# Optimization experiments

Hardware: AMD Instinct MI355X
Metric: run time of the kernel (lower is better)

## Reference

```python
import jax, jax.numpy as jnp
import numpy as np

D_MODEL = 1024
N_HEADS = 16
D_K = D_MODEL // N_HEADS


def setup_inputs() -> dict:
    key = jax.random.key(0)
    ks = jax.random.split(key, 11)
    B, S = 2, 2048
    scale = 0.02
    inp = {
        "q": jax.random.normal(ks[0], (B, S, D_MODEL), jnp.float32),
        "k": jax.random.normal(ks[1], (B, S, D_MODEL), jnp.float32),
        "v": jax.random.normal(ks[2], (B, S, D_MODEL), jnp.float32),
        "w_q": jax.random.normal(ks[3], (D_MODEL, D_MODEL), jnp.float32) * scale,
        "b_q": jnp.zeros((D_MODEL,), jnp.float32),
        "w_k": jax.random.normal(ks[4], (D_MODEL, D_MODEL), jnp.float32) * scale,
        "b_k": jnp.zeros((D_MODEL,), jnp.float32),
        "w_v": jax.random.normal(ks[5], (D_MODEL, D_MODEL), jnp.float32) * scale,
        "b_v": jnp.zeros((D_MODEL,), jnp.float32),
        "w_o": jax.random.normal(ks[6], (D_MODEL, D_MODEL), jnp.float32) * scale,
        "b_o": jnp.zeros((D_MODEL,), jnp.float32),
    }
    return inp


def reference(q, k, v, w_q, b_q, w_k, b_k, w_v, b_v, w_o, b_o):
    B, S, _ = q.shape
    # projections (torch Linear: x @ W.T + b); split into heads -> [B, H, S, d]
    def proj(x, w, b):
        return (x @ w.T + b).reshape(B, S, N_HEADS, D_K).transpose(0, 2, 1, 3)
    qh = proj(q, w_q, b_q)
    kh = proj(k, w_k, b_k)
    vh = proj(v, w_v, b_v)
    scores = jnp.einsum("bhqd,bhkd->bhqk", qh, kh) / jnp.sqrt(
        jnp.asarray(D_K, jnp.float32))
    attn = jax.nn.softmax(scores, axis=-1)  # dropout = identity (eval)
    out = jnp.einsum("bhqk,bhkd->bhqd", attn, vh)
    out = out.transpose(0, 2, 1, 3).reshape(B, S, D_MODEL)
    return out @ w_o.T + b_o
```

## Files before the change

kernel.cpp:

```cpp
#include <hip/hip_runtime.h>

typedef unsigned short u16;
typedef unsigned int u32;
typedef __attribute__((ext_vector_type(4))) unsigned short u16x4;
typedef __attribute__((ext_vector_type(8))) unsigned short u16x8;
typedef __attribute__((ext_vector_type(8))) __bf16 bf16x8;
typedef __attribute__((ext_vector_type(4))) float f32x4;
typedef __attribute__((ext_vector_type(16))) float f32x16;

#define SEQ 2048
#define DMODEL 1024
#define LDP 3072
#define MM (DMODEL * DMODEL)
#define SC 0.18033688f

__device__ __forceinline__ u16 f2bf(float f) {
  unsigned u = __builtin_bit_cast(unsigned, f);
  u = (u + 0x7fffu + ((u >> 16) & 1u)) >> 16;
  return (u16)u;
}

__device__ __forceinline__ u32 cvtpk(float lo, float hi) {
  u32 r;
  asm volatile("v_cvt_pk_bf16_f32 %0, %1, %2" : "=v"(r) : "v"(lo), "v"(hi));
  return r;
}

__device__ __forceinline__ float fexp2(float x) {
#if __has_builtin(__builtin_amdgcn_exp2f)
  return __builtin_amdgcn_exp2f(x);
#else
  return exp2f(x);
#endif
}

__device__ __forceinline__ bf16x8 ldbf8(const u16* p) {
  return __builtin_bit_cast(bf16x8, *(const u16x8*)p);
}
__device__ __forceinline__ bf16x8 ldbf8c(const char* p) {
  return __builtin_bit_cast(bf16x8, *(const u16x8*)p);
}

__device__ __forceinline__ f32x4 mfma16(bf16x8 a, bf16x8 b, f32x4 c) {
  return __builtin_amdgcn_mfma_f32_16x16x32_bf16(a, b, c, 0, 0, 0);
}
__device__ __forceinline__ f32x16 mfma32(bf16x8 a, bf16x8 b, f32x16 c) {
  return __builtin_amdgcn_mfma_f32_32x32x16_bf16(a, b, c, 0, 0, 0);
}

__device__ __forceinline__ void gl16(const void* g, void* l) {
  __builtin_amdgcn_global_load_lds(
      (__attribute__((address_space(1))) void*)(size_t)g,
      (__attribute__((address_space(3))) void*)l, 16, 0, 0);
}

__global__ void cast_all_k(const float* __restrict__ q, const float* __restrict__ k,
                           const float* __restrict__ v, const float* __restrict__ wq,
                           const float* __restrict__ wk, const float* __restrict__ wv,
                           const float* __restrict__ wo, u16* __restrict__ dq,
                           u16* __restrict__ dk, u16* __restrict__ dv,
                           u16* __restrict__ wqkv, u16* __restrict__ wob) {
  int b = blockIdx.x;
  const float* s;
  u16* d;
  if (b < 6144) {
    const int z = b >> 11;
    s = z == 0 ? q : z == 1 ? k : v;
    d = z == 0 ? dq : z == 1 ? dk : dv;
    b &= 2047;
  } else {
    const int z = (b - 6144) >> 9;
    s = z == 0 ? wq : z == 1 ? wk : z == 2 ? wv : wo;
    d = z < 3 ? wqkv + (size_t)z * MM : wob;
    b = (b - 6144) & 511;
  }
  const size_t i = ((size_t)b * blockDim.x + threadIdx.x) * 8;
  const float4 a = *(const float4*)(s + i);
  const float4 c = *(const float4*)(s + i + 4);
  u16x8 o;
  o[0] = f2bf(a.x); o[1] = f2bf(a.y); o[2] = f2bf(a.z); o[3] = f2bf(a.w);
  o[4] = f2bf(c.x); o[5] = f2bf(c.y); o[6] = f2bf(c.z); o[7] = f2bf(c.w);
  *(u16x8*)(d + i) = o;
}

template <int OMODE>
__device__ __forceinline__ void gemm_bt_body(const u16* __restrict__ A,
                                             const u16* __restrict__ Bw,
                                             const float* __restrict__ bias,
                                             void* __restrict__ Cv, const int K,
                                             const int ldc, const int ncol0,
                                             const int m0, const int n0,
                                             const float osc) {
  __shared__ u16 As[128 * 32];
  __shared__ u16 Bs[128 * 32];
  const int tid = threadIdx.x;
  const int lane = tid & 63;
  const int w = tid >> 6;
  const int l15 = lane & 15;
  const int lg = lane >> 4;

  f32x4 acc[4][4] = {};

  const int arow = (w >> 1) * 64 + l15;
  const int brow = (w & 1) * 64 + l15;
  const int kfb = lg * 16;

  const int strow = w * 32 + (lane >> 2);
  const u16* Ag = A + (size_t)(m0 + strow) * K + (lane & 3) * 8;
  const u16* Bg = Bw + (size_t)(n0 + strow) * K + (lane & 3) * 8;
  const size_t rstep = (size_t)16 * K;
  char* AsL0 = (char*)As + w * 32 * 64;
  char* AsL1 = AsL0 + 16 * 64;
  char* BsL0 = (char*)Bs + w * 32 * 64;
  char* BsL1 = BsL0 + 16 * 64;

  for (int k0 = 0; k0 < K; k0 += 32) {
    __syncthreads();
    gl16(Ag + k0, AsL0);
    gl16(Ag + k0 + rstep, AsL1);
    gl16(Bg + k0, BsL0);
    gl16(Bg + k0 + rstep, BsL1);
    __syncthreads();
    bf16x8 af[4], bfv[4];
#pragma unroll
    for (int t = 0; t < 4; ++t) {
      af[t] = ldbf8c((char*)As + (arow + t * 16) * 64 + kfb);
      bfv[t] = ldbf8c((char*)Bs + (brow + t * 16) * 64 + kfb);
    }
    __builtin_amdgcn_s_setprio(1);
#pragma unroll
    for (int i = 0; i < 4; ++i)
#pragma unroll
      for (int j = 0; j < 4; ++j) acc[i][j] = mfma16(af[i], bfv[j], acc[i][j]);
    __builtin_amdgcn_s_setprio(0);
  }

  const int mrow = (w >> 1) * 64 + lg * 4;
  const int ncol = (w & 1) * 64 + l15;
#pragma unroll
  for (int j = 0; j < 4; ++j) {
    const int gn = n0 + ncol + j * 16;
    const float bia = bias[gn];
#pragma unroll
    for (int i = 0; i < 4; ++i) {
      const int gmb = m0 + mrow + i * 16;
#pragma unroll
      for (int r = 0; r < 4; ++r) {
        const float val = (acc[i][j][r] + bia) * osc;
        const int gm = gmb + r;
        if (OMODE == 0) {
          ((float*)Cv)[(size_t)gm * ldc + gn] = val;
        } else if (OMODE == 1) {
          ((u16*)Cv)[(size_t)gm * ldc + ncol0 + gn] = f2bf(val);
        } else {
          const int bb = gm >> 11, ss = gm & 2047;
          const int hh = gn >> 6, dd = gn & 63;
          ((u16*)Cv)[(((size_t)(bb * 16 + hh) * 64 + dd) << 11) + ss] = f2bf(val);
        }
      }
    }
  }
}

__global__ __launch_bounds__(256, 3) void gemm_qkv_k(
    const u16* __restrict__ qb, const u16* __restrict__ kb,
    const u16* __restrict__ vb, const u16* __restrict__ wqkv,
    const float* __restrict__ bq, const float* __restrict__ bk,
    const float* __restrict__ bv, u16* __restrict__ proj, u16* __restrict__ vtb) {
  const int b = blockIdx.x;
  const int xcd = b & 7;
  const int i = b >> 3;
  const int z = i >> 5;
  const int j = i & 31;
  const int m0 = (xcd * 4 + (j >> 3)) * 128;
  const int n0 = (j & 7) * 128;
  if (z == 2)
    gemm_bt_body<2>(vb, wqkv + 2 * (size_t)MM, bv, vtb, DMODEL, 0, 0, m0, n0,
                    1.0f);
  else
    gemm_bt_body<1>(z == 0 ? qb : kb, wqkv + (size_t)z * MM, z == 0 ? bq : bk,
                    proj, DMODEL, LDP, z * DMODEL, m0, n0, z == 0 ? SC : 1.0f);
}

__global__ __launch_bounds__(256, 3) void gemm_o_k(const u16* __restrict__ attnb,
                                                   const u16* __restrict__ wob,
                                                   const float* __restrict__ bo,
                                                   float* __restrict__ out) {
  const int b = blockIdx.x;
  const int xcd = b & 7;
  const int i = b >> 3;
  const int m0 = (xcd * 4 + (i >> 3)) * 128;
  const int n0 = (i & 7) * 128;
  gemm_bt_body<0>(attnb, wob, bo, out, DMODEL, DMODEL, 0, m0, n0, 1.0f);
}

__global__ __launch_bounds__(256, 2) void attn_k(const u16* __restrict__ proj,
                                                 const u16* __restrict__ vtb,
                                                 u16* __restrict__ outa) {
  __shared__ u16 ks[2][64 * 64];
  __shared__ u16 vs[2][64 * 64];
  const int b = blockIdx.x;
  const int slot = b >> 3;
  const int bh = (b & 7) * 4 + (slot >> 4);
  const int qB = (slot & 15) * 128;
  const int tid = threadIdx.x;
  const int lane = tid & 63;
  const int w = tid >> 6;
  const size_t rb = (size_t)(bh >> 4) * SEQ;
  const int h = bh & 15;
  const int l31 = lane & 31;
  const int hi = lane >> 5;
  const int swzk = (l31 & 7) << 4;
  const int swzv = (l31 & 15) << 3;

  const u16* qp = proj + (rb + qB + w * 32 + l31) * LDP + h * 64 + hi * 8;
  bf16x8 qf[4];
#pragma unroll
  for (int km = 0; km < 4; ++km) qf[km] = ldbf8(qp + km * 16);

  const int srow = tid >> 2;
  const int scol = (tid & 3) * 32;
  const int scel = scol >> 1;
  const int kz0 = srow * 128 + (scol ^ ((srow & 7) << 4));
  const int kz1 = srow * 128 + ((scol + 16) ^ ((srow & 7) << 4));
  const int vz0 = srow * 128 + (scol ^ ((srow & 15) << 3));
  const int vz1 = srow * 128 + ((scol + 8) ^ ((srow & 15) << 3));
  const int vz2 = srow * 128 + ((scol + 16) ^ ((srow & 15) << 3));
  const int vz3 = srow * 128 + ((scol + 24) ^ ((srow & 15) << 3));
  const u16* kg = proj + rb * LDP + DMODEL + h * 64;
  const u16* vg = vtb + (size_t)bh * 64 * SEQ;

  u16x8 ka0, ka1, va0, va1;
  {
    const u16* kr = kg + (size_t)srow * LDP + scel;
    ka0 = *(const u16x8*)kr;
    ka1 = *(const u16x8*)(kr + 8);
    const u16* vr = vg + (size_t)srow * SEQ + scel;
    va0 = *(const u16x8*)vr;
    va1 = *(const u16x8*)(vr + 8);
  }

  f32x16 oa0 = {}, oa1 = {};
  float lrun = 0.f;
  int p = 0;

  for (int kv0 = 0; kv0 < SEQ; kv0 += 64) {
    {
      char* kd = (char*)ks[p];
      char* vd = (char*)vs[p];
      *(u16x8*)(kd + kz0) = ka0;
      *(u16x8*)(kd + kz1) = ka1;
      *(u16x4*)(vd + vz0) = *(u16x4*)&va0;
      *(u16x4*)(vd + vz1) = *((u16x4*)&va0 + 1);
      *(u16x4*)(vd + vz2) = *(u16x4*)&va1;
      *(u16x4*)(vd + vz3) = *((u16x4*)&va1 + 1);
    }
    __syncthreads();
    if (kv0 + 64 < SEQ) {
      const u16* kr = kg + (size_t)(kv0 + 64 + srow) * LDP + scel;
      ka0 = *(const u16x8*)kr;
      ka1 = *(const u16x8*)(kr + 8);
      const u16* vr = vg + (size_t)srow * SEQ + kv0 + 64 + scel;
      va0 = *(const u16x8*)vr;
      va1 = *(const u16x8*)(vr + 8);
    }
    const char* kp = (const char*)ks[p];
    const char* vp = (const char*)vs[p];
    f32x16 s0 = {}, s1 = {};
    __builtin_amdgcn_s_setprio(1);
#pragma unroll
    for (int km = 0; km < 4; ++km) {
      const int co = (km * 32 + hi * 16) ^ swzk;
      const bf16x8 k0 = ldbf8c(kp + l31 * 128 + co);
      const bf16x8 k1 = ldbf8c(kp + (32 + l31) * 128 + co);
      s0 = mfma32(k0, qf[km], s0);
      s1 = mfma32(k1, qf[km], s1);
    }
    __builtin_amdgcn_s_setprio(0);

#pragma unroll
    for (int r = 0; r < 16; ++r) s0[r] = fexp2(s0[r]);
#pragma unroll
    for (int r = 0; r < 16; ++r) s1[r] = fexp2(s1[r]);
    float rs = (((s0[0] + s0[1]) + (s0[2] + s0[3])) +
                ((s0[4] + s0[5]) + (s0[6] + s0[7]))) +
               (((s0[8] + s0[9]) + (s0[10] + s0[11])) +
                ((s0[12] + s0[13]) + (s0[14] + s0[15])));
    rs += (((s1[0] + s1[1]) + (s1[2] + s1[3])) +
           ((s1[4] + s1[5]) + (s1[6] + s1[7]))) +
          (((s1[8] + s1[9]) + (s1[10] + s1[11])) +
           ((s1[12] + s1[13]) + (s1[14] + s1[15])));
    rs += __shfl_xor(rs, 32);
    lrun += rs;

    __builtin_amdgcn_s_setprio(1);
#define PCHUNK(SV, G, CB)                                                \
    {                                                                    \
      u16x8 pbu;                                                         \
      ((u32*)&pbu)[0] = cvtpk(SV[G + 0], SV[G + 1]);                     \
      ((u32*)&pbu)[1] = cvtpk(SV[G + 2], SV[G + 3]);                     \
      ((u32*)&pbu)[2] = cvtpk(SV[G + 4], SV[G + 5]);                     \
      ((u32*)&pbu)[3] = cvtpk(SV[G + 6], SV[G + 7]);                     \
      const bf16x8 pb = __builtin_bit_cast(bf16x8, pbu);                 \
      const int vc0 = ((CB) + 8 * hi) ^ swzv;                            \
      const int vc1 = ((CB) + 16 + 8 * hi) ^ swzv;                       \
      const char* vr0 = vp + l31 * 128;                                  \
      const char* vr1 = vp + (32 + l31) * 128;                           \
      u16x8 vf0, vf1;                                                    \
      *(u16x4*)&vf0       = *(const u16x4*)(vr0 + vc0);                  \
      *((u16x4*)&vf0 + 1) = *(const u16x4*)(vr0 + vc1);                  \
      *(u16x4*)&vf1       = *(const u16x4*)(vr1 + vc0);                  \
      *((u16x4*)&vf1 + 1) = *(const u16x4*)(vr1 + vc1);                  \
      oa0 = mfma32(__builtin_bit_cast(bf16x8, vf0), pb, oa0);            \
      oa1 = mfma32(__builtin_bit_cast(bf16x8, vf1), pb, oa1);            \
    }
    PCHUNK(s0, 0, 0)
    PCHUNK(s0, 8, 32)
    PCHUNK(s1, 0, 64)
    PCHUNK(s1, 8, 96)
#undef PCHUNK
    __builtin_amdgcn_s_setprio(0);
    p ^= 1;
  }

  const float invl = 1.0f / lrun;
  u16* orow = outa + (rb + qB + w * 32 + l31) * DMODEL + h * 64 + hi * 4;
#pragma unroll
  for (int g = 0; g < 4; ++g) {
    u16x4 st0, st1;
    ((u32*)&st0)[0] = cvtpk(oa0[4 * g + 0] * invl, oa0[4 * g + 1] * invl);
    ((u32*)&st0)[1] = cvtpk(oa0[4 * g + 2] * invl, oa0[4 * g + 3] * invl);
    *(u16x4*)(orow + 8 * g) = st0;
    ((u32*)&st1)[0] = cvtpk(oa1[4 * g + 0] * invl, oa1[4 * g + 1] * invl);
    ((u32*)&st1)[1] = cvtpk(oa1[4 * g + 2] * invl, oa1[4 * g + 3] * invl);
    *(u16x4*)(orow + 32 + 8 * g) = st1;
  }
}

extern "C" void kernel_launch(void* const* d_in, const int* in_sizes, int n_in,
                              void* d_out, int out_size, void* d_ws, size_t ws_size,
                              hipStream_t stream) {
  const float* q  = (const float*)d_in[0];
  const float* k  = (const float*)d_in[1];
  const float* v  = (const float*)d_in[2];
  const float* wq = (const float*)d_in[3];
  const float* bq = (const float*)d_in[4];
  const float* wk = (const float*)d_in[5];
  const float* bk = (const float*)d_in[6];
  const float* wv = (const float*)d_in[7];
  const float* bv = (const float*)d_in[8];
  const float* wo = (const float*)d_in[9];
  const float* bo = (const float*)d_in[10];

  const size_t NTOK = (size_t)2 * SEQ;
  const size_t NELE = NTOK * DMODEL;
  u16* qb    = (u16*)d_ws;
  u16* kb    = qb + NELE;
  u16* vb    = kb + NELE;
  u16* wqkv  = vb + NELE;
  u16* wob   = wqkv + 3 * (size_t)MM;
  u16* projb = wob + (size_t)MM;
  u16* vtb   = projb + NTOK * LDP;
  u16* attnb = qb;

  cast_all_k<<<8192, 256, 0, stream>>>(q, k, v, wq, wk, wv, wo, qb, kb, vb,
                                       wqkv, wob);
  gemm_qkv_k<<<768, 256, 0, stream>>>(qb, kb, vb, wqkv, bq, bk, bv, projb, vtb);
  attn_k<<<512, 256, 0, stream>>>(projb, vtb, attnb);
  gemm_o_k<<<256, 256, 0, stream>>>(attnb, wob, bo, (float*)d_out);
}
```

Baseline: 120.9 us.

## Split KV range across two wave groups per attention block and merge partials

The attention block grows to 512 threads organised as two groups of four waves. Each group streams half of the key/value sequence through its own double-buffered shared-memory tiles. At the end, group 1 writes its unnormalised output accumulators and row sums to shared memory, and group 0 adds them in, normalises and stores. The aim is to double the waves working on each query tile and halve the serial KV loop length, which raises latency hiding. The costs are 64KB of shared memory per block and a tighter launch bound, which may limit residency or force register spills.

```diff
diff --git a/kernel.cpp b/kernel.cpp
--- a/kernel.cpp
+++ b/kernel.cpp
@@ -194,11 +194,10 @@
   gemm_bt_body<0>(attnb, wob, bo, out, DMODEL, DMODEL, 0, m0, n0, 1.0f);
 }
 
-__global__ __launch_bounds__(256, 2) void attn_k(const u16* __restrict__ proj,
+__global__ __launch_bounds__(512, 4) void attn_k(const u16* __restrict__ proj,
                                                  const u16* __restrict__ vtb,
                                                  u16* __restrict__ outa) {
-  __shared__ u16 ks[2][64 * 64];
-  __shared__ u16 vs[2][64 * 64];
+  __shared__ __align__(16) char smem[65536];
   const int b = blockIdx.x;
   const int slot = b >> 3;
   const int bh = (b & 7) * 4 + (slot >> 4);
@@ -206,6 +205,9 @@
   const int tid = threadIdx.x;
   const int lane = tid & 63;
   const int w = tid >> 6;
+  const int g = w >> 2;
+  const int wg = w & 3;
+  const int tg = tid & 255;
   const size_t rb = (size_t)(bh >> 4) * SEQ;
   const int h = bh & 15;
   const int l31 = lane & 31;
@@ -213,13 +215,16 @@
   const int swzk = (l31 & 7) << 4;
   const int swzv = (l31 & 15) << 3;
 
-  const u16* qp = proj + (rb + qB + w * 32 + l31) * LDP + h * 64 + hi * 8;
+  char* const ksb = smem + g * 32768;
+  char* const vsb = ksb + 16384;
+
+  const u16* qp = proj + (rb + qB + wg * 32 + l31) * LDP + h * 64 + hi * 8;
   bf16x8 qf[4];
 #pragma unroll
   for (int km = 0; km < 4; ++km) qf[km] = ldbf8(qp + km * 16);
 
-  const int srow = tid >> 2;
-  const int scol = (tid & 3) * 32;
+  const int srow = tg >> 2;
+  const int scol = (tg & 3) * 32;
   const int scel = scol >> 1;
   const int kz0 = srow * 128 + (scol ^ ((srow & 7) << 4));
   const int kz1 = srow * 128 + ((scol + 16) ^ ((srow & 7) << 4));
@@ -229,13 +234,14 @@
   const int vz3 = srow * 128 + ((scol + 24) ^ ((srow & 15) << 3));
   const u16* kg = proj + rb * LDP + DMODEL + h * 64;
   const u16* vg = vtb + (size_t)bh * 64 * SEQ;
+  const int kvbase = g * (SEQ / 2);
 
   u16x8 ka0, ka1, va0, va1;
   {
-    const u16* kr = kg + (size_t)srow * LDP + scel;
+    const u16* kr = kg + (size_t)(kvbase + srow) * LDP + scel;
     ka0 = *(const u16x8*)kr;
     ka1 = *(const u16x8*)(kr + 8);
-    const u16* vr = vg + (size_t)srow * SEQ + scel;
+    const u16* vr = vg + (size_t)srow * SEQ + kvbase + scel;
     va0 = *(const u16x8*)vr;
     va1 = *(const u16x8*)(vr + 8);
   }
@@ -244,10 +250,10 @@
   float lrun = 0.f;
   int p = 0;
 
-  for (int kv0 = 0; kv0 < SEQ; kv0 += 64) {
+  for (int it = 0; it < SEQ / 128; ++it) {
     {
-      char* kd = (char*)ks[p];
-      char* vd = (char*)vs[p];
+      char* kd = ksb + p * 8192;
+      char* vd = vsb + p * 8192;
       *(u16x8*)(kd + kz0) = ka0;
       *(u16x8*)(kd + kz1) = ka1;
       *(u16x4*)(vd + vz0) = *(u16x4*)&va0;
@@ -256,16 +262,17 @@
       *(u16x4*)(vd + vz3) = *((u16x4*)&va1 + 1);
     }
     __syncthreads();
-    if (kv0 + 64 < SEQ) {
-      const u16* kr = kg + (size_t)(kv0 + 64 + srow) * LDP + scel;
+    if (it + 1 < SEQ / 128) {
+      const int kvn = kvbase + (it + 1) * 64;
+      const u16* kr = kg + (size_t)(kvn + srow) * LDP + scel;
       ka0 = *(const u16x8*)kr;
       ka1 = *(const u16x8*)(kr + 8);
-      const u16* vr = vg + (size_t)srow * SEQ + kv0 + 64 + scel;
+      const u16* vr = vg + (size_t)srow * SEQ + kvn + scel;
       va0 = *(const u16x8*)vr;
       va1 = *(const u16x8*)(vr + 8);
     }
-    const char* kp = (const char*)ks[p];
-    const char* vp = (const char*)vs[p];
+    const char* kp = ksb + p * 8192;
+    const char* vp = vsb + p * 8192;
     f32x16 s0 = {}, s1 = {};
     __builtin_amdgcn_s_setprio(1);
 #pragma unroll
@@ -323,17 +330,37 @@
     p ^= 1;
   }
 
-  const float invl = 1.0f / lrun;
-  u16* orow = outa + (rb + qB + w * 32 + l31) * DMODEL + h * 64 + hi * 4;
-#pragma unroll
-  for (int g = 0; g < 4; ++g) {
-    u16x4 st0, st1;
-    ((u32*)&st0)[0] = cvtpk(oa0[4 * g + 0] * invl, oa0[4 * g + 1] * invl);
-    ((u32*)&st0)[1] = cvtpk(oa0[4 * g + 2] * invl, oa0[4 * g + 3] * invl);
-    *(u16x4*)(orow + 8 * g) = st0;
-    ((u32*)&st1)[0] = cvtpk(oa1[4 * g + 0] * invl, oa1[4 * g + 1] * invl);
-    ((u32*)&st1)[1] = cvtpk(oa1[4 * g + 2] * invl, oa1[4 * g + 3] * invl);
-    *(u16x4*)(orow + 32 + 8 * g) = st1;
+  float* sc = (float*)smem;
+  __syncthreads();
+  if (g == 1) {
+    const int col = wg * 64 + lane;
+#pragma unroll
+    for (int r = 0; r < 16; ++r) sc[r * 256 + col] = oa0[r];
+#pragma unroll
+    for (int r = 0; r < 16; ++r) sc[(16 + r) * 256 + col] = oa1[r];
+    sc[32 * 256 + col] = lrun;
+  }
+  __syncthreads();
+  if (g == 0) {
+    const int col = wg * 64 + lane;
+#pragma unroll
+    for (int r = 0; r < 16; ++r) oa0[r] += sc[r * 256 + col];
+#pragma unroll
+    for (int r = 0; r < 16; ++r) oa1[r] += sc[(16 + r) * 256 + col];
+    lrun += sc[32 * 256 + col];
+
+    const float invl = 1.0f / lrun;
+    u16* orow = outa + (rb + qB + wg * 32 + l31) * DMODEL + h * 64 + hi * 4;
+#pragma unroll
+    for (int gg = 0; gg < 4; ++gg) {
+      u16x4 st0, st1;
+      ((u32*)&st0)[0] = cvtpk(oa0[4 * gg + 0] * invl, oa0[4 * gg + 1] * invl);
+      ((u32*)&st0)[1] = cvtpk(oa0[4 * gg + 2] * invl, oa0[4 * gg + 3] * invl);
+      *(u16x4*)(orow + 8 * gg) = st0;
+      ((u32*)&st1)[0] = cvtpk(oa1[4 * gg + 0] * invl, oa1[4 * gg + 1] * invl);
+      ((u32*)&st1)[1] = cvtpk(oa1[4 * gg + 2] * invl, oa1[4 * gg + 3] * invl);
+      *(u16x4*)(orow + 32 + 8 * gg) = st1;
+    }
   }
 }
 
@@ -366,6 +393,6 @@
   cast_all_k<<<8192, 256, 0, stream>>>(q, k, v, wq, wk, wv, wo, qb, kb, vb,
                                        wqkv, wob);
   gemm_qkv_k<<<768, 256, 0, stream>>>(qb, kb, vb, wqkv, bq, bk, bv, projb, vtb);
-  attn_k<<<512, 256, 0, stream>>>(projb, vtb, attnb);
+  attn_k<<<512, 512, 0, stream>>>(projb, vtb, attnb);
   gemm_o_k<<<256, 256, 0, stream>>>(attnb, wob, bo, (float*)d_out);
 }
```

Result: slower. 183.8 us (+52.1%).
